# Kernel optimization log

Measured on AMD Instinct MI355X. Metric: run time of the kernel, lower is better.

The kernel has to match this reference:

```python
import jax, jax.numpy as jnp
import numpy as np

N_GRAPHS = 200
NODES_PER_GRAPH = 500
N_NODES = N_GRAPHS * NODES_PER_GRAPH  # 100000
N_EDGES = 1_600_000
INPUT_DIM = 64
GCN_DIM = 128
SEQ_LEN = 20
LSTM_DIM = 128
OUTPUT_DIM = 1


def setup_inputs() -> dict:
    key = jax.random.key(0)
    ks = jax.random.split(key, 10)
    # edges constrained to stay inside each graph (block-diagonal adjacency)
    src = jax.random.randint(ks[0], (N_EDGES,), 0, N_NODES, dtype=jnp.int32)
    dst_local = jax.random.randint(ks[1], (N_EDGES,), 0, NODES_PER_GRAPH, dtype=jnp.int32)
    dst = (src // NODES_PER_GRAPH) * NODES_PER_GRAPH + dst_local
    graph_ids = jnp.arange(N_NODES, dtype=jnp.int32) // NODES_PER_GRAPH
    x = jax.random.normal(ks[2], (N_NODES, INPUT_DIM), dtype=jnp.float32)
    s = 0.05
    w_gcn = jax.random.normal(ks[3], (INPUT_DIM, GCN_DIM), dtype=jnp.float32) * s
    b_gcn = jnp.zeros((GCN_DIM,), dtype=jnp.float32)
    w_ih = jax.random.normal(ks[4], (4 * LSTM_DIM, GCN_DIM), dtype=jnp.float32) * s
    w_hh = jax.random.normal(ks[5], (4 * LSTM_DIM, LSTM_DIM), dtype=jnp.float32) * s
    b_ih = jax.random.normal(ks[6], (4 * LSTM_DIM,), dtype=jnp.float32) * s
    b_hh = jax.random.normal(ks[7], (4 * LSTM_DIM,), dtype=jnp.float32) * s
    w_fc = jax.random.normal(ks[8], (OUTPUT_DIM, LSTM_DIM), dtype=jnp.float32) * s
    b_fc = jnp.zeros((OUTPUT_DIM,), dtype=jnp.float32)
    return {"x": x, "src": src, "dst": dst, "graph_ids": graph_ids,
            "w_gcn": w_gcn, "b_gcn": b_gcn, "w_ih": w_ih, "w_hh": w_hh,
            "b_ih": b_ih, "b_hh": b_hh, "w_fc": w_fc, "b_fc": b_fc}


def reference(x, src, dst, graph_ids, w_gcn, b_gcn, w_ih, w_hh, b_ih, b_hh, w_fc, b_fc):
    ones_e = jnp.ones((src.shape[0],), dtype=x.dtype)
    # DGL GraphConv norm='both': D_out^{-1/2} on src side, D_in^{-1/2} on dst side,
    # degrees clamped to min 1 (allow_zero_in_degree=True)
    out_deg = jnp.clip(jax.ops.segment_sum(ones_e, src, num_segments=N_NODES), 1.0)
    in_deg = jnp.clip(jax.ops.segment_sum(ones_e, dst, num_segments=N_NODES), 1.0)
    h = x * (out_deg ** -0.5)[:, None]                               # [N, Din]
    agg = jax.ops.segment_sum(h[src], dst, num_segments=N_NODES)     # gather+scatter-add
    h = agg * (in_deg ** -0.5)[:, None]
    h = jnp.maximum(h @ w_gcn + b_gcn, 0.0)                           # [N, GCN_DIM], ReLU
    # dgl.mean_nodes: per-graph mean pool
    cnt = jax.ops.segment_sum(jnp.ones((N_NODES,), h.dtype), graph_ids, num_segments=N_GRAPHS)
    hg = jax.ops.segment_sum(h, graph_ids, num_segments=N_GRAPHS) / cnt[:, None]  # [T, D]
    # build_dataset: sliding windows of length SEQ_LEN over the graph time series
    B = N_GRAPHS - SEQ_LEN + 1
    idx = jnp.arange(B)[:, None] + jnp.arange(SEQ_LEN)[None, :]
    dat = hg[idx]                                                      # [B, L, D]
    # single-layer LSTM (PyTorch gate order i,f,g,o), zero initial state
    x_proj = jnp.einsum('bld,gd->blg', dat, w_ih) + b_ih               # [B, L, 4H]
    h0 = jnp.zeros((B, LSTM_DIM), dat.dtype)
    c0 = jnp.zeros((B, LSTM_DIM), dat.dtype)

    def step(carry, xt):
        hprev, cprev = carry
        gates = xt + hprev @ w_hh.T + b_hh
        i, f, g, o = jnp.split(gates, 4, axis=-1)
        c = jax.nn.sigmoid(f) * cprev + jax.nn.sigmoid(i) * jnp.tanh(g)
        hh = jax.nn.sigmoid(o) * jnp.tanh(c)
        return (hh, c), None

    (h_n, _), _ = jax.lax.scan(step, (h0, c0), jnp.swapaxes(x_proj, 0, 1))
    pred = h_n @ w_fc.T + b_fc                                         # [B, OUTPUT_DIM]
    return pred
```

## Files before the change

### kernel.cpp

```cpp
#include <hip/hip_runtime.h>
#include <hip/hip_bf16.h>

#define N_GRAPHS 200
#define NPG      500
#define NPGP     512
#define N_NODES_ 100000
#define N_EDGES_ 1600000
#define DIN      64
#define DG       128
#define SEQ      20
#define HL       128
#define G4       512
#define BWIN     (N_GRAPHS - SEQ + 1)
#define NPART    512
#define EPB      (N_EDGES_/NPART)
#define SLOTS    48
#define CAP      9216

typedef __attribute__((ext_vector_type(8))) short short8;
typedef __attribute__((ext_vector_type(4))) float float4v;
typedef __attribute__((ext_vector_type(2))) _Float16 half2v;

__device__ __forceinline__ float sigmoidf_(float v){ return 1.0f/(1.0f+expf(-v)); }

__device__ __forceinline__ unsigned short f2bf(float f) {
  unsigned int u = __float_as_uint(f);
  u += 0x7fffu + ((u >> 16) & 1u);
  return (unsigned short)(u >> 16);
}

__device__ __forceinline__ float h2dot(half2v a, half2v b, float c) {
#if __has_builtin(__builtin_amdgcn_fdot2)
  return __builtin_amdgcn_fdot2(a, b, c, false);
#else
  return c + (float)a.x*(float)b.x + (float)a.y*(float)b.y;
#endif
}

__global__ __launch_bounds__(256) void k_part(const int* __restrict__ src,
                                              const int* __restrict__ dst,
                                              const float* __restrict__ w_hh,
                                              int* __restrict__ gcount,
                                              int* __restrict__ part,
                                              int4* __restrict__ whh16) {
  __shared__ int cnt[N_GRAPHS];
  __shared__ int base[N_GRAPHS];
  __shared__ int buf[N_GRAPHS][SLOTS];
  int b = blockIdx.x, t = threadIdx.x;
  if (b < 32) {
    int i = b*256 + t;
    int k4 = i >> 9, r = i & 511;
    const float4* wp = (const float4*)(w_hh + (size_t)r*HL + k4*8);
    float4 w0 = wp[0], w1 = wp[1];
    half2v p0 = {(_Float16)w0.x, (_Float16)w0.y};
    half2v p1 = {(_Float16)w0.z, (_Float16)w0.w};
    half2v p2 = {(_Float16)w1.x, (_Float16)w1.y};
    half2v p3 = {(_Float16)w1.z, (_Float16)w1.w};
    int4 pk;
    pk.x = __builtin_bit_cast(int, p0); pk.y = __builtin_bit_cast(int, p1);
    pk.z = __builtin_bit_cast(int, p2); pk.w = __builtin_bit_cast(int, p3);
    whh16[i] = pk;
  }
  for (int g = t; g < N_GRAPHS; g += 256) cnt[g] = 0;
  __syncthreads();
  int e0 = b*EPB;
  for (int i = t; i < EPB; i += 256) {
    int s = src[e0+i], d = dst[e0+i];
    int g = s / NPG;
    int pk = ((s - g*NPG) << 9) | (d - g*NPG);
    int pos = atomicAdd(&cnt[g], 1);
    if (pos < SLOTS) buf[g][pos] = pk;
    else { int gp = atomicAdd(&gcount[g], 1); part[g*CAP + gp] = pk; }
  }
  __syncthreads();
  if (t < N_GRAPHS) base[t] = atomicAdd(&gcount[t], min(cnt[t], SLOTS));
  __syncthreads();
  int w = t >> 6, lane = t & 63;
  for (int g = w; g < N_GRAPHS; g += 4) {
    int n = min(cnt[g], SLOTS);
    if (lane < n) part[g*CAP + base[g] + lane] = buf[g][lane];
  }
}

__global__ __launch_bounds__(1024) void k_graph(
    const int* __restrict__ gcount, const int* __restrict__ part,
    const float* __restrict__ x,
    const float* __restrict__ w_gcn, const float* __restrict__ b_gcn,
    const float* __restrict__ w_ih,  const float* __restrict__ b_ih,
    float* __restrict__ proj) {
  __shared__ int meta[2048];
  __shared__ int wsum[8];
  __shared__ __align__(16) float hgS[DG];
  __shared__ unsigned short sorted[CAP];
  __shared__ __align__(16) int4 xs[4008];
  __shared__ __align__(16) int4 hpre[4096];
  int* indeg  = meta;
  int* outdeg = meta + 512;
  int* off    = meta + 1024;
  float* soS  = (float*)(meta + 1536);
  int g = blockIdx.x, t = threadIdx.x;
  int lane = t & 63, w = t >> 6;

  float4 wg[2];
  #pragma unroll
  for (int q = 0; q < 2; ++q) wg[q] = ((const float4*)w_gcn)[t + q*1024];

  meta[t] = 0; meta[t + 1024] = 0;
  __syncthreads();
  int nseg = gcount[g], seg0 = g*CAP;
  int pr[9];
  #pragma unroll
  for (int q = 0; q < 9; ++q) {
    int e = t + q*1024;
    pr[q] = (e < nseg) ? part[seg0 + e] : -1;
  }
  #pragma unroll
  for (int q = 0; q < 9; ++q) {
    int p = pr[q];
    if (p >= 0) {
      atomicAdd(&indeg[p & 511], 1);
      atomicAdd(&outdeg[p >> 9], 1);
    }
  }
  __syncthreads();
  if (t < 512) {
    int v = indeg[t], sc = v;
    #pragma unroll
    for (int o = 1; o < 64; o <<= 1) { int nn = __shfl_up(sc, o); if (lane >= o) sc += nn; }
    if (lane == 63) wsum[t >> 6] = sc;
    __syncthreads();
    int woff = 0;
    #pragma unroll
    for (int i = 0; i < 8; ++i) woff += (i < (t >> 6)) ? wsum[i] : 0;
    off[t] = woff + sc - v;
    soS[t] = rsqrtf((float)max(outdeg[t], 1));
  } else {
    __syncthreads();
  }
  __syncthreads();
  const float4* xg = ((const float4*)x) + (size_t)g*8000;
  ushort4* xd = (ushort4*)xs;
  for (int i = t; i < 8000; i += 1024) {
    float4 vv = xg[i];
    float s2 = soS[i >> 4];
    ushort4 u;
    u.x = f2bf(vv.x*s2); u.y = f2bf(vv.y*s2); u.z = f2bf(vv.z*s2); u.w = f2bf(vv.w*s2);
    xd[i] = u;
  }
  if (t < 16) xd[8000 + t] = make_ushort4(0,0,0,0);
  #pragma unroll
  for (int q = 0; q < 9; ++q) {
    int p = pr[q];
    if (p >= 0) {
      int pos = atomicAdd(&off[p & 511], 1);
      sorted[pos] = (unsigned short)(p >> 9);
    }
  }
  __syncthreads();
  int g8 = lane >> 3, fl = lane & 7;
  int G = w*8 + g8;
  for (int sI = 0; sI < 4; ++sI) {
    int nl = sI*128 + G;
    int4 outv = make_int4(0,0,0,0);
    if (nl < NPG) {
      int end = off[nl], dgr = indeg[nl], st = end - dgr;
      float aHi[4] = {0.f,0.f,0.f,0.f};
      float aLo[4] = {0.f,0.f,0.f,0.f};
      int ev = (fl < dgr) ? (int)sorted[st + fl] : 500;
      for (int c0 = 0; c0 < dgr; c0 += 8) {
        int nc = c0 + 8;
        int evn = (nc + fl < dgr) ? (int)sorted[st + nc + fl] : 500;
        #pragma unroll
        for (int j = 0; j < 8; ++j) {
          int se = __shfl(ev, (g8 << 3) + j);
          int4 vv = xs[(se << 3) + fl];
          aHi[0] += __uint_as_float((unsigned)vv.x & 0xffff0000u);
          aLo[0] += __uint_as_float((unsigned)vv.x << 16);
          aHi[1] += __uint_as_float((unsigned)vv.y & 0xffff0000u);
          aLo[1] += __uint_as_float((unsigned)vv.y << 16);
          aHi[2] += __uint_as_float((unsigned)vv.z & 0xffff0000u);
          aLo[2] += __uint_as_float((unsigned)vv.z << 16);
          aHi[3] += __uint_as_float((unsigned)vv.w & 0xffff0000u);
          aLo[3] += __uint_as_float((unsigned)vv.w << 16);
        }
        ev = evn;
      }
      float sn = rsqrtf((float)max(dgr, 1));
      outv.x = (int)(((unsigned)f2bf(aLo[0]*sn)) | ((unsigned)f2bf(aHi[0]*sn) << 16));
      outv.y = (int)(((unsigned)f2bf(aLo[1]*sn)) | ((unsigned)f2bf(aHi[1]*sn) << 16));
      outv.z = (int)(((unsigned)f2bf(aLo[2]*sn)) | ((unsigned)f2bf(aHi[2]*sn) << 16));
      outv.w = (int)(((unsigned)f2bf(aLo[3]*sn)) | ((unsigned)f2bf(aHi[3]*sn) << 16));
    }
    hpre[(nl << 3) + (fl ^ (nl & 7))] = outv;
  }
  __syncthreads();
  unsigned short* wLds = (unsigned short*)sorted;
  #pragma unroll
  for (int q = 0; q < 2; ++q) {
    int i = t + q*1024;
    int k = i >> 5, c4 = (i & 31) << 2;
    int h = k >> 5, j = k & 7, lhi = ((k >> 3) & 3) << 4;
    float vvv[4] = {wg[q].x, wg[q].y, wg[q].z, wg[q].w};
    #pragma unroll
    for (int u = 0; u < 4; ++u) {
      int n = c4 + u;
      int idx = ((n >> 4)*2 + h)*64 + lhi + (n & 15);
      wLds[idx*8 + j] = f2bf(vvv[u]);
    }
  }
  __syncthreads();
  float* pS = (float*)meta;
  int quad = lane >> 4, l15 = lane & 15;
  float bcol[8];
  #pragma unroll
  for (int nt = 0; nt < 8; ++nt) bcol[nt] = b_gcn[nt*16 + l15];
  float psum[8] = {0.f,0.f,0.f,0.f,0.f,0.f,0.f,0.f};
  #pragma unroll
  for (int i = 0; i < 2; ++i) {
    int row0 = (w + 16*i) << 4;
    int r = row0 + l15;
    int4 a0i = hpre[(r << 3) + (quad ^ (r & 7))];
    int4 a1i = hpre[(r << 3) + ((quad + 4) ^ (r & 7))];
    short8 a0 = *(const short8*)&a0i;
    short8 a1 = *(const short8*)&a1i;
    #pragma unroll
    for (int nt = 0; nt < 8; ++nt) {
      short8 b0 = *((const short8*)&wLds[((nt*2+0)*64 + lane)*8]);
      short8 b1 = *((const short8*)&wLds[((nt*2+1)*64 + lane)*8]);
      float4v acc = {0.f, 0.f, 0.f, 0.f};
      acc = __builtin_amdgcn_mfma_f32_16x16x32_bf16(a0, b0, acc, 0, 0, 0);
      acc = __builtin_amdgcn_mfma_f32_16x16x32_bf16(a1, b1, acc, 0, 0, 0);
      #pragma unroll
      for (int r4 = 0; r4 < 4; ++r4) {
        int node = row0 + quad*4 + r4;
        float vvv = acc[r4] + bcol[nt];
        psum[nt] += (node < NPG) ? fmaxf(vvv, 0.f) : 0.f;
      }
    }
  }
  #pragma unroll
  for (int nt = 0; nt < 8; ++nt) {
    float vvv = psum[nt];
    vvv += __shfl_xor(vvv, 16);
    vvv += __shfl_xor(vvv, 32);
    if (lane < 16) pS[w*DG + nt*16 + lane] = vvv;
  }
  __syncthreads();
  if (t < DG) {
    float sum = 0.f;
    #pragma unroll
    for (int w16 = 0; w16 < 16; ++w16) sum += pS[w16*DG + t];
    hgS[t] = sum * (1.0f/NPG);
  }
  __syncthreads();
  {
    int r = t >> 1, half = t & 1;
    const float4* wr = (const float4*)(w_ih + (size_t)r*HL) + half*16;
    const float4* hv = (const float4*)hgS + half*16;
    float acc = half ? 0.f : b_ih[r];
    #pragma unroll
    for (int k4 = 0; k4 < 16; ++k4) {
      float4 w4 = wr[k4]; float4 h4 = hv[k4];
      acc += w4.x*h4.x + w4.y*h4.y + w4.z*h4.z + w4.w*h4.w;
    }
    acc += __shfl_xor(acc, 1);
    if (!half) proj[(size_t)g*G4 + r] = acc;
  }
}

__global__ __launch_bounds__(512) void k_lstm(const float* __restrict__ proj,
    const int4* __restrict__ whh16, const float* __restrict__ b_hh,
    const float* __restrict__ w_fc, const float* __restrict__ b_fc,
    float* __restrict__ out) {
  __shared__ float gS[G4];
  __shared__ __align__(16) int4 hPi[16];
  __shared__ float fcS[2];
  int b = blockIdx.x, t = threadIdx.x;
  int4 W[16];
  #pragma unroll
  for (int k4 = 0; k4 < 16; ++k4) W[k4] = whh16[(k4 << 9) + t];
  if (t < 16) hPi[t] = make_int4(0,0,0,0);
  float bh = b_hh[t];
  float c = 0.f;
  __syncthreads();
  for (int l = 0; l < SEQ; ++l) {
    float a0 = proj[(size_t)(b+l)*G4 + t] + bh;
    float a1 = 0.f, a2 = 0.f, a3 = 0.f;
    #pragma unroll
    for (int k4 = 0; k4 < 16; k4 += 4) {
      int4 hv0 = hPi[k4+0]; int4 hv1 = hPi[k4+1];
      int4 hv2 = hPi[k4+2]; int4 hv3 = hPi[k4+3];
      a0 = h2dot(__builtin_bit_cast(half2v, W[k4+0].x), __builtin_bit_cast(half2v, hv0.x), a0);
      a0 = h2dot(__builtin_bit_cast(half2v, W[k4+0].y), __builtin_bit_cast(half2v, hv0.y), a0);
      a0 = h2dot(__builtin_bit_cast(half2v, W[k4+0].z), __builtin_bit_cast(half2v, hv0.z), a0);
      a0 = h2dot(__builtin_bit_cast(half2v, W[k4+0].w), __builtin_bit_cast(half2v, hv0.w), a0);
      a1 = h2dot(__builtin_bit_cast(half2v, W[k4+1].x), __builtin_bit_cast(half2v, hv1.x), a1);
      a1 = h2dot(__builtin_bit_cast(half2v, W[k4+1].y), __builtin_bit_cast(half2v, hv1.y), a1);
      a1 = h2dot(__builtin_bit_cast(half2v, W[k4+1].z), __builtin_bit_cast(half2v, hv1.z), a1);
      a1 = h2dot(__builtin_bit_cast(half2v, W[k4+1].w), __builtin_bit_cast(half2v, hv1.w), a1);
      a2 = h2dot(__builtin_bit_cast(half2v, W[k4+2].x), __builtin_bit_cast(half2v, hv2.x), a2);
      a2 = h2dot(__builtin_bit_cast(half2v, W[k4+2].y), __builtin_bit_cast(half2v, hv2.y), a2);
      a2 = h2dot(__builtin_bit_cast(half2v, W[k4+2].z), __builtin_bit_cast(half2v, hv2.z), a2);
      a2 = h2dot(__builtin_bit_cast(half2v, W[k4+2].w), __builtin_bit_cast(half2v, hv2.w), a2);
      a3 = h2dot(__builtin_bit_cast(half2v, W[k4+3].x), __builtin_bit_cast(half2v, hv3.x), a3);
      a3 = h2dot(__builtin_bit_cast(half2v, W[k4+3].y), __builtin_bit_cast(half2v, hv3.y), a3);
      a3 = h2dot(__builtin_bit_cast(half2v, W[k4+3].z), __builtin_bit_cast(half2v, hv3.z), a3);
      a3 = h2dot(__builtin_bit_cast(half2v, W[k4+3].w), __builtin_bit_cast(half2v, hv3.w), a3);
    }
    gS[t] = (a0 + a1) + (a2 + a3);
    __syncthreads();
    if (t < 128) {
      float iv = sigmoidf_(gS[t]);
      float fv = sigmoidf_(gS[HL + t]);
      float gv = tanhf(gS[2*HL + t]);
      float ov = sigmoidf_(gS[3*HL + t]);
      c = fv*c + iv*gv;
      float h = ov * tanhf(c);
      float hp2 = __shfl_xor(h, 1);
      if (!(t & 1)) {
        half2v hp = {(_Float16)h, (_Float16)hp2};
        ((int*)hPi)[t >> 1] = __builtin_bit_cast(int, hp);
      }
      if (l == SEQ-1) {
        float s = h * w_fc[t];
        #pragma unroll
        for (int o = 32; o > 0; o >>= 1) s += __shfl_down(s, o);
        if ((t & 63) == 0) fcS[t >> 6] = s;
      }
    }
    __syncthreads();
  }
  if (t == 0) out[b] = fcS[0] + fcS[1] + b_fc[0];
}

extern "C" void kernel_launch(void* const* d_in, const int* in_sizes, int n_in,
                              void* d_out, int out_size, void* d_ws, size_t ws_size,
                              hipStream_t stream) {
  const float* x     = (const float*)d_in[0];
  const int*   src   = (const int*)d_in[1];
  const int*   dst   = (const int*)d_in[2];
  const float* w_gcn = (const float*)d_in[4];
  const float* b_gcn = (const float*)d_in[5];
  const float* w_ih  = (const float*)d_in[6];
  const float* w_hh  = (const float*)d_in[7];
  const float* b_ih  = (const float*)d_in[8];
  const float* b_hh  = (const float*)d_in[9];
  const float* w_fc  = (const float*)d_in[10];
  const float* b_fc  = (const float*)d_in[11];
  float* out = (float*)d_out;

  char* ws = (char*)d_ws;
  size_t off = 0;
  auto alloc = [&](size_t bytes) -> void* {
    void* p = ws + off; off += (bytes + 255) & ~(size_t)255; return p;
  };
  int* gcount  = (int*)alloc((size_t)N_GRAPHS*4);
  int* part    = (int*)alloc((size_t)N_GRAPHS*CAP*4);
  int4* whh16  = (int4*)alloc((size_t)8192*16);
  float* proj  = (float*)alloc((size_t)N_GRAPHS*G4*4);
  (void)ws_size; (void)in_sizes; (void)n_in; (void)out_size;

  hipMemsetAsync(gcount, 0, (size_t)N_GRAPHS*4, stream);
  k_part<<<NPART, 256, 0, stream>>>(src, dst, w_hh, gcount, part, whh16);
  k_graph<<<N_GRAPHS, 1024, 0, stream>>>(gcount, part, x, w_gcn, b_gcn, w_ih, b_ih, proj);
  k_lstm<<<BWIN, 512, 0, stream>>>(proj, whh16, b_hh, w_fc, b_fc, out);
}
```

Measured before the change: 171.4 us.

## Retune edge partitioning, add dynamic node queue, prefetch LSTM inputs, fast transcendentals

Edge partitioning now runs as 256 blocks of 1024 threads with int2 vectorized loads and more local slots per graph. The graph kernel replaces its fixed node assignment with an LDS atomic work queue so that 8-lane groups can balance uneven in-degrees. The LSTM kernel prefetches all projection inputs into registers before the recurrence and switches to fast __expf-based sigmoid and tanh. The intent is to cut partition overhead, aggregation load imbalance and serial-step latency, at the cost of slightly lower transcendental accuracy and more register pressure.

```diff
diff --git a/kernel.cpp b/kernel.cpp
--- a/kernel.cpp
+++ b/kernel.cpp
@@ -12,16 +12,20 @@
 #define HL       128
 #define G4       512
 #define BWIN     (N_GRAPHS - SEQ + 1)
-#define NPART    512
+#define NPART    256
 #define EPB      (N_EDGES_/NPART)
-#define SLOTS    48
+#define SLOTS    64
 #define CAP      9216
 
 typedef __attribute__((ext_vector_type(8))) short short8;
 typedef __attribute__((ext_vector_type(4))) float float4v;
 typedef __attribute__((ext_vector_type(2))) _Float16 half2v;
 
-__device__ __forceinline__ float sigmoidf_(float v){ return 1.0f/(1.0f+expf(-v)); }
+__device__ __forceinline__ float sigmoidf_(float v){ return 1.0f/(1.0f+__expf(-v)); }
+__device__ __forceinline__ float tanhf_(float x){
+  float e = __expf(2.0f*x);
+  return 1.0f - 2.0f/(e + 1.0f);
+}
 
 __device__ __forceinline__ unsigned short f2bf(float f) {
   unsigned int u = __float_as_uint(f);
@@ -37,18 +41,18 @@
 #endif
 }
 
-__global__ __launch_bounds__(256) void k_part(const int* __restrict__ src,
-                                              const int* __restrict__ dst,
-                                              const float* __restrict__ w_hh,
-                                              int* __restrict__ gcount,
-                                              int* __restrict__ part,
-                                              int4* __restrict__ whh16) {
+__global__ __launch_bounds__(1024) void k_part(const int* __restrict__ src,
+                                               const int* __restrict__ dst,
+                                               const float* __restrict__ w_hh,
+                                               int* __restrict__ gcount,
+                                               int* __restrict__ part,
+                                               int4* __restrict__ whh16) {
   __shared__ int cnt[N_GRAPHS];
   __shared__ int base[N_GRAPHS];
   __shared__ int buf[N_GRAPHS][SLOTS];
   int b = blockIdx.x, t = threadIdx.x;
-  if (b < 32) {
-    int i = b*256 + t;
+  if (b < 8) {
+    int i = b*1024 + t;
     int k4 = i >> 9, r = i & 511;
     const float4* wp = (const float4*)(w_hh + (size_t)r*HL + k4*8);
     float4 w0 = wp[0], w1 = wp[1];
@@ -61,22 +65,33 @@
     pk.z = __builtin_bit_cast(int, p2); pk.w = __builtin_bit_cast(int, p3);
     whh16[i] = pk;
   }
-  for (int g = t; g < N_GRAPHS; g += 256) cnt[g] = 0;
+  if (t < N_GRAPHS) cnt[t] = 0;
   __syncthreads();
   int e0 = b*EPB;
-  for (int i = t; i < EPB; i += 256) {
-    int s = src[e0+i], d = dst[e0+i];
-    int g = s / NPG;
-    int pk = ((s - g*NPG) << 9) | (d - g*NPG);
-    int pos = atomicAdd(&cnt[g], 1);
-    if (pos < SLOTS) buf[g][pos] = pk;
-    else { int gp = atomicAdd(&gcount[g], 1); part[g*CAP + gp] = pk; }
+  const int2* s2 = (const int2*)(src + e0);
+  const int2* d2 = (const int2*)(dst + e0);
+  for (int i = t; i < EPB/2; i += 1024) {
+    int2 ss = s2[i], dd = d2[i];
+    {
+      int g = ss.x / NPG;
+      int pk = ((ss.x - g*NPG) << 9) | (dd.x - g*NPG);
+      int pos = atomicAdd(&cnt[g], 1);
+      if (pos < SLOTS) buf[g][pos] = pk;
+      else { int gp = atomicAdd(&gcount[g], 1); part[g*CAP + gp] = pk; }
+    }
+    {
+      int g = ss.y / NPG;
+      int pk = ((ss.y - g*NPG) << 9) | (dd.y - g*NPG);
+      int pos = atomicAdd(&cnt[g], 1);
+      if (pos < SLOTS) buf[g][pos] = pk;
+      else { int gp = atomicAdd(&gcount[g], 1); part[g*CAP + gp] = pk; }
+    }
   }
   __syncthreads();
   if (t < N_GRAPHS) base[t] = atomicAdd(&gcount[t], min(cnt[t], SLOTS));
   __syncthreads();
   int w = t >> 6, lane = t & 63;
-  for (int g = w; g < N_GRAPHS; g += 4) {
+  for (int g = w; g < N_GRAPHS; g += 16) {
     int n = min(cnt[g], SLOTS);
     if (lane < n) part[g*CAP + base[g] + lane] = buf[g][lane];
   }
@@ -90,6 +105,7 @@
     float* __restrict__ proj) {
   __shared__ int meta[2048];
   __shared__ int wsum[8];
+  __shared__ int qhead;
   __shared__ __align__(16) float hgS[DG];
   __shared__ unsigned short sorted[CAP];
   __shared__ __align__(16) int4 xs[4008];
@@ -123,19 +139,20 @@
     }
   }
   __syncthreads();
+  int vscan = 0, scscan = 0;
   if (t < 512) {
-    int v = indeg[t], sc = v;
-    #pragma unroll
-    for (int o = 1; o < 64; o <<= 1) { int nn = __shfl_up(sc, o); if (lane >= o) sc += nn; }
-    if (lane == 63) wsum[t >> 6] = sc;
-    __syncthreads();
+    vscan = indeg[t]; scscan = vscan;
+    #pragma unroll
+    for (int o = 1; o < 64; o <<= 1) { int nn = __shfl_up(scscan, o); if (lane >= o) scscan += nn; }
+    if (lane == 63) wsum[w] = scscan;
+  }
+  __syncthreads();
+  if (t < 512) {
     int woff = 0;
     #pragma unroll
-    for (int i = 0; i < 8; ++i) woff += (i < (t >> 6)) ? wsum[i] : 0;
-    off[t] = woff + sc - v;
+    for (int i = 0; i < 8; ++i) woff += (i < w) ? wsum[i] : 0;
+    off[t] = woff + scscan - vscan;
     soS[t] = rsqrtf((float)max(outdeg[t], 1));
-  } else {
-    __syncthreads();
   }
   __syncthreads();
   const float4* xg = ((const float4*)x) + (size_t)g*8000;
@@ -156,11 +173,11 @@
       sorted[pos] = (unsigned short)(p >> 9);
     }
   }
+  if (t == 0) qhead = 128;
   __syncthreads();
   int g8 = lane >> 3, fl = lane & 7;
-  int G = w*8 + g8;
-  for (int sI = 0; sI < 4; ++sI) {
-    int nl = sI*128 + G;
+  int nl = w*8 + g8;
+  while (nl < 512) {
     int4 outv = make_int4(0,0,0,0);
     if (nl < NPG) {
       int end = off[nl], dgr = indeg[nl], st = end - dgr;
@@ -192,6 +209,9 @@
       outv.w = (int)(((unsigned)f2bf(aLo[3]*sn)) | ((unsigned)f2bf(aHi[3]*sn) << 16));
     }
     hpre[(nl << 3) + (fl ^ (nl & 7))] = outv;
+    int nxt = 0;
+    if (fl == 0) nxt = atomicAdd(&qhead, 1);
+    nl = __shfl(nxt, (g8 << 3));
   }
   __syncthreads();
   unsigned short* wLds = (unsigned short*)sorted;
@@ -276,6 +296,9 @@
   __shared__ __align__(16) int4 hPi[16];
   __shared__ float fcS[2];
   int b = blockIdx.x, t = threadIdx.x;
+  float pj[SEQ];
+  #pragma unroll
+  for (int l = 0; l < SEQ; ++l) pj[l] = proj[(size_t)(b+l)*G4 + t];
   int4 W[16];
   #pragma unroll
   for (int k4 = 0; k4 < 16; ++k4) W[k4] = whh16[(k4 << 9) + t];
@@ -283,8 +306,9 @@
   float bh = b_hh[t];
   float c = 0.f;
   __syncthreads();
+  #pragma unroll
   for (int l = 0; l < SEQ; ++l) {
-    float a0 = proj[(size_t)(b+l)*G4 + t] + bh;
+    float a0 = pj[l] + bh;
     float a1 = 0.f, a2 = 0.f, a3 = 0.f;
     #pragma unroll
     for (int k4 = 0; k4 < 16; k4 += 4) {
@@ -312,10 +336,10 @@
     if (t < 128) {
       float iv = sigmoidf_(gS[t]);
       float fv = sigmoidf_(gS[HL + t]);
-      float gv = tanhf(gS[2*HL + t]);
+      float gv = tanhf_(gS[2*HL + t]);
       float ov = sigmoidf_(gS[3*HL + t]);
       c = fv*c + iv*gv;
-      float h = ov * tanhf(c);
+      float h = ov * tanhf_(c);
       float hp2 = __shfl_xor(h, 1);
       if (!(t & 1)) {
         half2v hp = {(_Float16)h, (_Float16)hp2};
@@ -361,7 +385,7 @@
   (void)ws_size; (void)in_sizes; (void)n_in; (void)out_size;
 
   hipMemsetAsync(gcount, 0, (size_t)N_GRAPHS*4, stream);
-  k_part<<<NPART, 256, 0, stream>>>(src, dst, w_hh, gcount, part, whh16);
+  k_part<<<NPART, 1024, 0, stream>>>(src, dst, w_hh, gcount, part, whh16);
   k_graph<<<N_GRAPHS, 1024, 0, stream>>>(gcount, part, x, w_gcn, b_gcn, w_ih, b_ih, proj);
   k_lstm<<<BWIN, 512, 0, stream>>>(proj, whh16, b_hh, w_fc, b_fc, out);
 }
```

New measurement: 154.5 us. -9.8%, faster.
